# Kernel tuning notes

Measured on AMD Instinct MI355X. Metric: run time of the kernel, lower is better.

The kernel has to match this reference:

```python
import jax, jax.numpy as jnp
import numpy as np

NJ, COL, TMP = 24, 14, 3
LENGS = np.array([[[0, 1], [5, 6]], [[1, 2], [6, 7]], [[2, 3], [7, 8]], [[2, 4], [7, 9]],
                  [[15, 16], [19, 20]], [[16, 17], [20, 21]], [[17, 18], [21, 22]],
                  [[0, 23], [5, 23]], [[15, 23], [19, 23]]])


def setup_inputs() -> dict:
    key = jax.random.key(0)
    ks = jax.random.split(key, 8)
    B = 4096
    o2D = jax.random.normal(ks[0], (B, 2 * NJ, COL, COL), jnp.float32)
    o3D = jax.random.normal(ks[1], (B, 3 * NJ, COL, COL), jnp.float32)
    h = jax.random.normal(ks[2], (B, NJ, COL, COL), jnp.float32)
    d = jnp.where(jax.random.uniform(ks[3], (B,)) < 0.05, -1000.0,
                  jax.random.normal(ks[4], (B,), jnp.float32))
    t2D = jax.random.uniform(ks[5], (B, NJ, 2), jnp.float32)   # targets in [0,1)
    t3D = jax.random.normal(ks[6], (B, NJ, 3), jnp.float32)
    vj = (jax.random.uniform(ks[7], (B, NJ)) < 0.9).astype(jnp.float32)
    v = jnp.broadcast_to(vj[:, :, None], (B, NJ, 3)) + 0.0  # 0/1, equal across last dim
    return {"o2D": o2D, "o3D": o3D, "h": h, "d": d, "t2D": t2D, "t3D": t3D, "v": v}


def reference(o2D, o3D, h, d, t2D, t3D, v):
    B = h.shape[0]
    scale = 1.0 / COL

    # argmax over each joint heatmap -> integer coords
    argmax = jnp.argmax(h.reshape(B, NJ, COL * COL), axis=-1)  # [B,Nj]
    yC = argmax // COL
    xC = argmax % COL
    bi = jnp.arange(B)[:, None]
    ji = jnp.arange(NJ)[None, :]

    # gather offset maps at argmax locations, add discretized coord
    x2D = jnp.stack([o2D[bi, ji, yC, xC] + xC.astype(jnp.float32) * scale,
                     o2D[bi, ji + NJ, yC, xC] + yC.astype(jnp.float32) * scale], axis=-1)  # [B,Nj,2]
    x3D_full = jnp.stack([o3D[bi, ji, yC, xC] + xC.astype(jnp.float32) * scale,
                          o3D[bi, ji + NJ, yC, xC] + yC.astype(jnp.float32) * scale,
                          o3D[bi, ji + 2 * NJ, yC, xC]], axis=-1)  # [B,Nj,3]
    d_ok = (d > -990.0)[:, None, None]  # rows with valid depth
    x3D = jnp.where(d_ok, x3D_full, 0.0)  # invalid-depth rows keep zeros (as original)

    # target gaussian heatmap placement + out-of-bounds visibility pruning
    vis = v[:, :, 0] == 1.0  # [B,Nj]
    mu = jnp.floor(t2D * COL + 0.5).astype(jnp.int32)  # int() trunc == floor for t2D>=0
    mu_x, mu_y = mu[..., 0], mu[..., 1]
    ul_x, ul_y = mu_x - TMP, mu_y - TMP
    br_x, br_y = mu_x + TMP + 1, mu_y + TMP + 1
    oob = vis & ((ul_x >= COL) | (ul_y >= COL) | (br_x <= 0) | (br_y <= 0))  # [B,Nj]
    v_new = jnp.where(oob[:, :, None], 0.0, v)  # v[i,j,:]=0 on oob
    # v3D row zeroed if depth invalid or any joint in row was oob
    v3D = jnp.where(d_ok & ~jnp.any(oob, axis=1)[:, None, None], v, 0.0)

    # separable clipped 7x7 gaussian: exp(-((x-mu_x)^2+(y-mu_y)^2)/2) inside |.|<=3
    xs = jnp.arange(COL)
    dx = xs[None, None, :] - mu_x[:, :, None]  # [B,Nj,col]
    dy = xs[None, None, :] - mu_y[:, :, None]
    gx = jnp.exp(-0.5 * dx.astype(jnp.float32) ** 2) * (jnp.abs(dx) <= TMP)
    gy = jnp.exp(-0.5 * dy.astype(jnp.float32) ** 2) * (jnp.abs(dy) <= TMP)
    place = (vis & ~oob).astype(jnp.float32)
    tt = gy[:, :, :, None] * gx[:, :, None, :] * place[:, :, None, None]  # [B,Nj,col,col]

    # d1: masked heatmap MSE, normalized by count of visible joints
    mask1 = (v_new[:, :, 0] != 0.0)
    diff1 = (h - tt) * mask1[:, :, None, None].astype(h.dtype)
    cnt = jnp.sum(mask1.astype(jnp.float32))
    d1 = jnp.sum(diff1 * diff1) / cnt

    # d2: masked 2D coord MSE
    diff2 = (x2D - t2D) * v_new[:, :, :2]
    N2 = jnp.sum(v_new) / 3.0
    d2 = jnp.sum(diff2 * diff2) / N2

    # d3: masked 3D coord MSE
    diff3 = (x3D - t3D) * v3D
    N3 = jnp.sum(v3D) / 3.0
    d3 = jnp.sum(diff3 * diff3) / N3

    # d4: limb-length symmetry penalty over 9 limb pairs
    ll = jnp.float32(0.0)
    lengV = jnp.float32(0.0)
    for k in range(LENGS.shape[0]):
        i00, i01 = int(LENGS[k, 0, 0]), int(LENGS[k, 0, 1])
        i10, i11 = int(LENGS[k, 1, 0]), int(LENGS[k, 1, 1])
        vv = v_new[:, i00] * v_new[:, i01] * v_new[:, i10] * v_new[:, i11]  # [B,3]
        le0 = (x3D[:, i00] - x3D[:, i01]) * vv
        le1 = (x3D[:, i10] - x3D[:, i11]) * vv
        le0s = jnp.sqrt(jnp.sum(le0 * le0))
        le1s = jnp.sqrt(jnp.sum(le1 * le1))
        dleng = le0s - le1s
        lengV = lengV + jnp.sum(vv) / 3.0
        ll = ll + dleng * dleng
    d4 = ll / lengV

    return d1 + d2 + d3 + d4
```

## Files before the change

### kernel.cpp

```cpp
#include <hip/hip_runtime.h>
#include <math.h>

#define NJ 24
#define COLN 14
#define MAPSZ 196
#define ROW (NJ*MAPSZ)
#define NACC 25
#define TMPW 3

__device__ __constant__ int c_lengs[9][2][2] = {
  {{0,1},{5,6}}, {{1,2},{6,7}}, {{2,3},{7,8}}, {{2,4},{7,9}},
  {{15,16},{19,20}}, {{16,17},{20,21}}, {{17,18},{21,22}},
  {{0,23},{5,23}}, {{15,23},{19,23}}
};

__global__ __launch_bounds__(256) void loss_main(
    const float* __restrict__ o2D, const float* __restrict__ o3D,
    const float* __restrict__ h,   const float* __restrict__ dpt,
    const float* __restrict__ t2D, const float* __restrict__ t3D,
    const float* __restrict__ v,   float* __restrict__ partials, int B)
{
  __shared__ float sh[ROW];
  __shared__ float s_gx[NJ][COLN];
  __shared__ float s_gy[NJ][COLN];
  __shared__ int   s_mux[NJ], s_muy[NJ];
  __shared__ float s_v[NJ], s_vnew[NJ], s_place[NJ];
  __shared__ int   s_oob[NJ];
  __shared__ float s_t2d[NJ][2];
  __shared__ float s_t3d[NJ][3];
  __shared__ float s_x3d[NJ][3];
  __shared__ float s_jd2[NJ], s_jd3[NJ];
  __shared__ float s_limb0[9], s_limb1[9], s_vv[9];
  __shared__ float s_red[256];
  __shared__ float s_out[NACC];
  __shared__ int   s_anyoob;
  __shared__ int   s_dok;

  const int b   = blockIdx.x;
  const int tid = threadIdx.x;

  if (tid < NJ) {
    int j = tid;
    float tx = t2D[((size_t)b*NJ + j)*2 + 0];
    float ty = t2D[((size_t)b*NJ + j)*2 + 1];
    float v0 = v[((size_t)b*NJ + j)*3 + 0];
    s_t2d[j][0] = tx; s_t2d[j][1] = ty;
    s_t3d[j][0] = t3D[((size_t)b*NJ + j)*3 + 0];
    s_t3d[j][1] = t3D[((size_t)b*NJ + j)*3 + 1];
    s_t3d[j][2] = t3D[((size_t)b*NJ + j)*3 + 2];
    s_v[j] = v0;
    int mux = (int)floorf(__fadd_rn(__fmul_rn(tx, 14.0f), 0.5f));
    int muy = (int)floorf(__fadd_rn(__fmul_rn(ty, 14.0f), 0.5f));
    s_mux[j] = mux; s_muy[j] = muy;
    bool vis = (v0 == 1.0f);
    bool oob = vis && ((mux - TMPW >= COLN) || (muy - TMPW >= COLN) ||
                       (mux + TMPW + 1 <= 0) || (muy + TMPW + 1 <= 0));
    s_oob[j]   = oob ? 1 : 0;
    s_vnew[j]  = oob ? 0.0f : v0;
    s_place[j] = (vis && !oob) ? 1.0f : 0.0f;
  }
  if (tid == 0) s_dok = (dpt[b] > -990.0f) ? 1 : 0;
  {
    const float4* hp  = (const float4*)(h + (size_t)b * ROW);
    float4*       shp = (float4*)sh;
    for (int i = tid; i < ROW/4; i += 256) shp[i] = hp[i];
  }
  __syncthreads();

  for (int i = tid; i < NJ*COLN; i += 256) {
    int j = i / COLN, x = i - j*COLN;
    int dx = x - s_mux[j];
    int dy = x - s_muy[j];
    s_gx[j][x] = (dx >= -TMPW && dx <= TMPW) ? expf(-0.5f * (float)(dx*dx)) : 0.0f;
    s_gy[j][x] = (dy >= -TMPW && dy <= TMPW) ? expf(-0.5f * (float)(dy*dy)) : 0.0f;
  }
  if (tid == 0) {
    int a = 0;
    #pragma unroll
    for (int j = 0; j < NJ; ++j) a |= s_oob[j];
    s_anyoob = a;
  }
  __syncthreads();

  float g0=0.f,g1=0.f,g2=0.f,g3=0.f,g4=0.f;
  int   jj = -1, yC = 0, xC = 0;
  if (tid < NJ*8) {
    int j = tid >> 3, p = tid & 7;
    float best = -INFINITY; int bidx = 0;
    const float* hj = sh + j*MAPSZ;
    for (int idx = p; idx < MAPSZ; idx += 8) {
      float val = hj[idx];
      if (val > best) { best = val; bidx = idx; }
    }
    #pragma unroll
    for (int m = 1; m < 8; m <<= 1) {
      float ov = __shfl_xor(best, m);
      int   oi = __shfl_xor(bidx, m);
      if (ov > best || (ov == best && oi < bidx)) { best = ov; bidx = oi; }
    }
    if (p == 0) {
      jj = j;
      yC = bidx / COLN; xC = bidx - yC*COLN;
      size_t o2base = ((size_t)b*2*NJ + j)*MAPSZ + bidx;
      size_t o3base = ((size_t)b*3*NJ + j)*MAPSZ + bidx;
      g0 = o2D[o2base];
      g1 = o2D[o2base + (size_t)NJ*MAPSZ];
      g2 = o3D[o3base];
      g3 = o3D[o3base + (size_t)NJ*MAPSZ];
      g4 = o3D[o3base + (size_t)2*NJ*MAPSZ];
    }
  }

  float local1 = 0.0f;
  for (int i = tid; i < ROW; i += 256) {
    int j = i / MAPSZ;
    int r = i - j*MAPSZ;
    int y = r / COLN;
    int x = r - y*COLN;
    float tt   = s_gy[j][y] * s_gx[j][x];
    float diff = sh[i] - tt;
    local1 += s_place[j] * diff * diff;
  }

  if (jj >= 0) {
    const float sc = 1.0f/14.0f;
    float x2_0 = g0 + (float)xC * sc;
    float x2_1 = g1 + (float)yC * sc;
    float dok  = s_dok ? 1.0f : 0.0f;
    float x3_0 = (g2 + (float)xC * sc) * dok;
    float x3_1 = (g3 + (float)yC * sc) * dok;
    float x3_2 = g4 * dok;
    s_x3d[jj][0] = x3_0; s_x3d[jj][1] = x3_1; s_x3d[jj][2] = x3_2;
    float vn  = s_vnew[jj];
    float d20 = (x2_0 - s_t2d[jj][0]) * vn;
    float d21 = (x2_1 - s_t2d[jj][1]) * vn;
    s_jd2[jj] = d20*d20 + d21*d21;
    float v3 = (s_dok && !s_anyoob) ? s_v[jj] : 0.0f;
    float e0 = (x3_0 - s_t3d[jj][0]) * v3;
    float e1 = (x3_1 - s_t3d[jj][1]) * v3;
    float e2 = (x3_2 - s_t3d[jj][2]) * v3;
    s_jd3[jj] = e0*e0 + e1*e1 + e2*e2;
  }
  __syncthreads();

  if (tid < 9) {
    int k = tid;
    int i00 = c_lengs[k][0][0], i01 = c_lengs[k][0][1];
    int i10 = c_lengs[k][1][0], i11 = c_lengs[k][1][1];
    float vv = s_vnew[i00]*s_vnew[i01]*s_vnew[i10]*s_vnew[i11];
    float S0 = 0.f, S1 = 0.f;
    #pragma unroll
    for (int c = 0; c < 3; ++c) {
      float l0 = (s_x3d[i00][c] - s_x3d[i01][c]) * vv;
      float l1 = (s_x3d[i10][c] - s_x3d[i11][c]) * vv;
      S0 += l0*l0; S1 += l1*l1;
    }
    s_limb0[k] = S0; s_limb1[k] = S1; s_vv[k] = vv;
  }
  s_red[tid] = local1;
  __syncthreads();
  #pragma unroll
  for (int s = 128; s > 0; s >>= 1) {
    if (tid < s) s_red[tid] += s_red[tid + s];
    __syncthreads();
  }

  if (tid == 0) {
    float sum2 = 0.f, N2 = 0.f, sum3 = 0.f, cnt = 0.f, Nv = 0.f, lengV = 0.f;
    #pragma unroll
    for (int j = 0; j < NJ; ++j) {
      sum2 += s_jd2[j]; N2 += s_vnew[j]; sum3 += s_jd3[j];
      cnt += s_place[j]; Nv += s_v[j];
    }
    float N3 = (s_dok && !s_anyoob) ? Nv : 0.0f;
    #pragma unroll
    for (int k = 0; k < 9; ++k) lengV += s_vv[k];
    s_out[0] = s_red[0];
    s_out[1] = cnt;
    s_out[2] = sum2;
    s_out[3] = N2;
    s_out[4] = sum3;
    s_out[5] = N3;
    s_out[6] = lengV;
    #pragma unroll
    for (int k = 0; k < 9; ++k) {
      s_out[7+k]  = s_limb0[k];
      s_out[16+k] = s_limb1[k];
    }
  }
  __syncthreads();
  if (tid < NACC) partials[(size_t)tid*B + b] = s_out[tid];
}

__global__ __launch_bounds__(256) void loss_reduce(
    const float* __restrict__ partials, float* __restrict__ out, int B)
{
  __shared__ double s_acc[NACC];
  int tid = threadIdx.x;
  int wave = tid >> 6, lane = tid & 63;
  for (int a = wave; a < NACC; a += 4) {
    double s = 0.0;
    for (int i = lane; i < B; i += 64) s += (double)partials[(size_t)a*B + i];
    #pragma unroll
    for (int m = 32; m >= 1; m >>= 1) s += __shfl_down(s, m);
    if (lane == 0) s_acc[a] = s;
  }
  __syncthreads();
  if (tid == 0) {
    double d1 = s_acc[0] / s_acc[1];
    double d2 = s_acc[2] / s_acc[3];
    double d3 = s_acc[4] / s_acc[5];
    double ll = 0.0;
    #pragma unroll
    for (int k = 0; k < 9; ++k) {
      double dl = sqrt(s_acc[7+k]) - sqrt(s_acc[16+k]);
      ll += dl*dl;
    }
    double d4 = ll / s_acc[6];
    out[0] = (float)(d1 + d2 + d3 + d4);
  }
}

extern "C" void kernel_launch(void* const* d_in, const int* in_sizes, int n_in,
                              void* d_out, int out_size, void* d_ws, size_t ws_size,
                              hipStream_t stream) {
  const float* o2D = (const float*)d_in[0];
  const float* o3D = (const float*)d_in[1];
  const float* h   = (const float*)d_in[2];
  const float* dpt = (const float*)d_in[3];
  const float* t2D = (const float*)d_in[4];
  const float* t3D = (const float*)d_in[5];
  const float* v   = (const float*)d_in[6];
  const int B = in_sizes[3];
  float* partials = (float*)d_ws;
  float* out = (float*)d_out;

  loss_main<<<B, 256, 0, stream>>>(o2D, o3D, h, dpt, t2D, t3D, v, partials, B);
  loss_reduce<<<1, 256, 0, stream>>>(partials, out, B);
}
```

Measured before the change: 503.6 us.

## Use async global-to-LDS loads, constant gaussians, wave-shuffle reduction, fewer barriers

Loads the heatmap row with global_load_lds directly into shared memory, so the per-joint setup can run while the load is still in flight. The gaussian table is now built from a constant lookup instead of expf, and the out-of-bounds flag comes from a ballot, which removes one barrier phase. The d1 loop is restructured so each of 196 threads walks the joints without integer division. The tree reduction is replaced by wave shuffles plus a four-entry shared array, removing eight barriers. The risks are that 60 threads sit idle in the d1 loop and that the hand-written vmcnt wait must correctly fence the asynchronous LDS loads.

New measurement: 498.9 us. About the same (-0.9%).

```diff
diff --git a/kernel.cpp b/kernel.cpp
--- a/kernel.cpp
+++ b/kernel.cpp
@@ -13,6 +13,15 @@
   {{15,16},{19,20}}, {{16,17},{20,21}}, {{17,18},{21,22}},
   {{0,23},{5,23}}, {{15,23},{19,23}}
 };
+
+__device__ __forceinline__ float gauss_of(int ad) {
+  float g = 0.0f;
+  g = (ad == 3) ? (float)0.011108996538242306 : g;
+  g = (ad == 2) ? (float)0.1353352832366127   : g;
+  g = (ad == 1) ? (float)0.6065306597126334   : g;
+  g = (ad == 0) ? 1.0f                        : g;
+  return g;
+}
 
 __global__ __launch_bounds__(256) void loss_main(
     const float* __restrict__ o2D, const float* __restrict__ o3D,
@@ -23,63 +32,73 @@
   __shared__ float sh[ROW];
   __shared__ float s_gx[NJ][COLN];
   __shared__ float s_gy[NJ][COLN];
-  __shared__ int   s_mux[NJ], s_muy[NJ];
   __shared__ float s_v[NJ], s_vnew[NJ], s_place[NJ];
-  __shared__ int   s_oob[NJ];
   __shared__ float s_t2d[NJ][2];
   __shared__ float s_t3d[NJ][3];
   __shared__ float s_x3d[NJ][3];
   __shared__ float s_jd2[NJ], s_jd3[NJ];
   __shared__ float s_limb0[9], s_limb1[9], s_vv[9];
-  __shared__ float s_red[256];
+  __shared__ float s_red4[4];
   __shared__ float s_out[NACC];
   __shared__ int   s_anyoob;
   __shared__ int   s_dok;
 
-  const int b   = blockIdx.x;
-  const int tid = threadIdx.x;
-
-  if (tid < NJ) {
-    int j = tid;
-    float tx = t2D[((size_t)b*NJ + j)*2 + 0];
-    float ty = t2D[((size_t)b*NJ + j)*2 + 1];
-    float v0 = v[((size_t)b*NJ + j)*3 + 0];
-    s_t2d[j][0] = tx; s_t2d[j][1] = ty;
-    s_t3d[j][0] = t3D[((size_t)b*NJ + j)*3 + 0];
-    s_t3d[j][1] = t3D[((size_t)b*NJ + j)*3 + 1];
-    s_t3d[j][2] = t3D[((size_t)b*NJ + j)*3 + 2];
-    s_v[j] = v0;
-    int mux = (int)floorf(__fadd_rn(__fmul_rn(tx, 14.0f), 0.5f));
-    int muy = (int)floorf(__fadd_rn(__fmul_rn(ty, 14.0f), 0.5f));
-    s_mux[j] = mux; s_muy[j] = muy;
-    bool vis = (v0 == 1.0f);
-    bool oob = vis && ((mux - TMPW >= COLN) || (muy - TMPW >= COLN) ||
-                       (mux + TMPW + 1 <= 0) || (muy + TMPW + 1 <= 0));
-    s_oob[j]   = oob ? 1 : 0;
-    s_vnew[j]  = oob ? 0.0f : v0;
-    s_place[j] = (vis && !oob) ? 1.0f : 0.0f;
-  }
-  if (tid == 0) s_dok = (dpt[b] > -990.0f) ? 1 : 0;
+  const int b    = blockIdx.x;
+  const int tid  = threadIdx.x;
+  const int lane = tid & 63;
+  const int w    = tid >> 6;
+
   {
-    const float4* hp  = (const float4*)(h + (size_t)b * ROW);
-    float4*       shp = (float4*)sh;
-    for (int i = tid; i < ROW/4; i += 256) shp[i] = hp[i];
-  }
-  __syncthreads();
-
-  for (int i = tid; i < NJ*COLN; i += 256) {
-    int j = i / COLN, x = i - j*COLN;
-    int dx = x - s_mux[j];
-    int dy = x - s_muy[j];
-    s_gx[j][x] = (dx >= -TMPW && dx <= TMPW) ? expf(-0.5f * (float)(dx*dx)) : 0.0f;
-    s_gy[j][x] = (dy >= -TMPW && dy <= TMPW) ? expf(-0.5f * (float)(dy*dy)) : 0.0f;
-  }
-  if (tid == 0) {
-    int a = 0;
-    #pragma unroll
-    for (int j = 0; j < NJ; ++j) a |= s_oob[j];
-    s_anyoob = a;
-  }
+    const float* hrow = h + (size_t)b * ROW;
+    #pragma unroll
+    for (int k = 0; k < 4; ++k) {
+      int base = k*1024 + w*256;
+      __builtin_amdgcn_global_load_lds(
+        (const __attribute__((address_space(1))) void*)(hrow + base + lane*4),
+        (__attribute__((address_space(3))) void*)(&sh[base]), 16, 0, 0);
+    }
+    int base = 4096 + w*256;
+    if (base + lane*4 < ROW) {
+      __builtin_amdgcn_global_load_lds(
+        (const __attribute__((address_space(1))) void*)(hrow + base + lane*4),
+        (__attribute__((address_space(3))) void*)(&sh[base]), 16, 0, 0);
+    }
+  }
+
+  if (tid == 64) s_dok = (dpt[b] > -990.0f) ? 1 : 0;
+
+  if (w == 0) {
+    bool oob = false;
+    if (tid < NJ) {
+      int j = tid;
+      float tx = t2D[((size_t)b*NJ + j)*2 + 0];
+      float ty = t2D[((size_t)b*NJ + j)*2 + 1];
+      float v0 = v[((size_t)b*NJ + j)*3 + 0];
+      s_t2d[j][0] = tx; s_t2d[j][1] = ty;
+      s_t3d[j][0] = t3D[((size_t)b*NJ + j)*3 + 0];
+      s_t3d[j][1] = t3D[((size_t)b*NJ + j)*3 + 1];
+      s_t3d[j][2] = t3D[((size_t)b*NJ + j)*3 + 2];
+      s_v[j] = v0;
+      int mux = (int)floorf(__fadd_rn(__fmul_rn(tx, 14.0f), 0.5f));
+      int muy = (int)floorf(__fadd_rn(__fmul_rn(ty, 14.0f), 0.5f));
+      bool vis = (v0 == 1.0f);
+      oob = vis && ((mux - TMPW >= COLN) || (muy - TMPW >= COLN) ||
+                    (mux + TMPW + 1 <= 0) || (muy + TMPW + 1 <= 0));
+      s_vnew[j]  = oob ? 0.0f : v0;
+      s_place[j] = (vis && !oob) ? 1.0f : 0.0f;
+      #pragma unroll
+      for (int x = 0; x < COLN; ++x) {
+        int dx = x - mux; int adx = dx < 0 ? -dx : dx;
+        int dy = x - muy; int ady = dy < 0 ? -dy : dy;
+        s_gx[j][x] = gauss_of(adx);
+        s_gy[j][x] = gauss_of(ady);
+      }
+    }
+    unsigned long long m = __ballot(oob);
+    if (lane == 0) s_anyoob = (m != 0ull) ? 1 : 0;
+  }
+
+  asm volatile("s_waitcnt vmcnt(0)" ::: "memory");
   __syncthreads();
 
   float g0=0.f,g1=0.f,g2=0.f,g3=0.f,g4=0.f;
@@ -112,14 +131,14 @@
   }
 
   float local1 = 0.0f;
-  for (int i = tid; i < ROW; i += 256) {
-    int j = i / MAPSZ;
-    int r = i - j*MAPSZ;
-    int y = r / COLN;
-    int x = r - y*COLN;
-    float tt   = s_gy[j][y] * s_gx[j][x];
-    float diff = sh[i] - tt;
-    local1 += s_place[j] * diff * diff;
+  if (tid < MAPSZ) {
+    int y = tid / COLN, x = tid - y*COLN;
+    #pragma unroll
+    for (int j = 0; j < NJ; ++j) {
+      float tt   = s_gy[j][y] * s_gx[j][x];
+      float diff = sh[j*MAPSZ + tid] - tt;
+      local1 += s_place[j] * diff * diff;
+    }
   }
 
   if (jj >= 0) {
@@ -157,13 +176,10 @@
     }
     s_limb0[k] = S0; s_limb1[k] = S1; s_vv[k] = vv;
   }
-  s_red[tid] = local1;
-  __syncthreads();
   #pragma unroll
-  for (int s = 128; s > 0; s >>= 1) {
-    if (tid < s) s_red[tid] += s_red[tid + s];
-    __syncthreads();
-  }
+  for (int m = 1; m < 64; m <<= 1) local1 += __shfl_xor(local1, m);
+  if (lane == 0) s_red4[w] = local1;
+  __syncthreads();
 
   if (tid == 0) {
     float sum2 = 0.f, N2 = 0.f, sum3 = 0.f, cnt = 0.f, Nv = 0.f, lengV = 0.f;
@@ -175,7 +191,7 @@
     float N3 = (s_dok && !s_anyoob) ? Nv : 0.0f;
     #pragma unroll
     for (int k = 0; k < 9; ++k) lengV += s_vv[k];
-    s_out[0] = s_red[0];
+    s_out[0] = s_red4[0] + s_red4[1] + s_red4[2] + s_red4[3];
     s_out[1] = cnt;
     s_out[2] = sum2;
     s_out[3] = N2;
```
